# Kernel tuning notes

Hardware: AMD Instinct MI355X
Metric: run time of the kernel (lower is better)

The kernel has to match this reference:

```python
import jax, jax.numpy as jnp
import numpy as np

N = 50000   # nodes
E = 600000  # edges (avg degree ~12)
R = 8       # num_relations = 2 * n_speakers**2, n_speakers=2
B = 32      # num_bases = args.batch_size
GD, H1, H2 = 128, 128, 128


def setup_inputs() -> dict:
    key = jax.random.key(0)
    ks = jax.random.split(key, 16)
    w = lambda k, shape: jax.random.normal(k, shape, jnp.float32) * 0.05
    return {
        "node_features": jax.random.normal(ks[0], (N, GD), jnp.float32),
        "edge_index": jax.random.randint(ks[1], (2, E), 0, N),
        "edge_norm": jax.random.uniform(ks[2], (E,), jnp.float32),
        "edge_type": jax.random.randint(ks[3], (E,), 0, R),
        "basis": w(ks[4], (B, GD, H1)),
        "comp": w(ks[5], (R, B)),
        "root": w(ks[6], (GD, H1)),
        "bias1": jnp.zeros((H1,), jnp.float32),
        "w_key": w(ks[7], (H1, H2)),
        "b_key": jnp.zeros((H2,), jnp.float32),
        "w_query": w(ks[8], (H1, H2)),
        "b_query": jnp.zeros((H2,), jnp.float32),
        "w_value": w(ks[9], (H1, H2)),
        "b_value": jnp.zeros((H2,), jnp.float32),
        "w_skip": w(ks[10], (H1, H2)),
        "b_skip": jnp.zeros((H2,), jnp.float32),
    }


def reference(node_features, edge_index, edge_norm, edge_type, basis, comp,
              root, bias1, w_key, b_key, w_query, b_query, w_value, b_value,
              w_skip, b_skip):
    n = node_features.shape[0]
    r = comp.shape[0]
    src, dst = edge_index[0], edge_index[1]

    # ---- RGCNConv (basis decomposition, per-relation mean aggregation) ----
    W = jnp.einsum('rb,bio->rio', comp, basis)            # [R, GD, H1]
    xW = jnp.einsum('ni,rio->rno', node_features, W)      # [R, N, H1]
    msg = xW[edge_type, src]                              # [E, H1]
    seg = edge_type * n + dst                             # combined (relation, dst) segment id
    agg = jax.ops.segment_sum(msg, seg, num_segments=r * n).reshape(r, n, -1)
    cnt = jax.ops.segment_sum(jnp.ones(msg.shape[0], jnp.float32), seg,
                              num_segments=r * n).reshape(r, n, 1)
    h = (agg / jnp.maximum(cnt, 1.0)).sum(0) + node_features @ root + bias1

    # ---- ResGatedGraphConv: sigmoid(k_i + q_j) * v_j, sum-aggregated + skip ----
    k = h @ w_key + b_key
    q = h @ w_query + b_query
    v = h @ w_value + b_value
    m = jax.nn.sigmoid(k[dst] + q[src]) * v[src]          # [E, H2]
    out = jax.ops.segment_sum(m, dst, num_segments=n) + h @ w_skip + b_skip
    return out
```

## Files before the change

### kernel.cpp

```cpp
#include <hip/hip_runtime.h>
#include <stdint.h>

#define GD 128
#define H1 128
#define H2 128
#define NBASES 32
#define NREL 8
#define KA 1152

typedef __attribute__((ext_vector_type(8))) short bf16x8;
typedef __attribute__((ext_vector_type(4))) float f32x4;

static inline size_t align256(size_t x){ return (x + 255) & ~(size_t)255; }

__device__ __forceinline__ float bf2f(uint32_t u16){
  union { uint32_t u; float f; } c; c.u = (u16 & 0xffffu) << 16; return c.f;
}
__device__ __forceinline__ unsigned short f2bf(float f){
  union { float f; uint32_t u; } c; c.f = f;
  uint32_t u = c.u;
  u += 0x7fffu + ((u >> 16) & 1u);
  return (unsigned short)(u >> 16);
}
__device__ __forceinline__ uint32_t pkbf(float a, float b){
  union { float f; uint32_t u; } ca, cb; ca.f = a; cb.f = b;
  return __builtin_amdgcn_perm(cb.u + 0x8000u, ca.u + 0x8000u, 0x07060302u);
}
__device__ __forceinline__ float rdlanef(float v, int l){
  return __int_as_float(__builtin_amdgcn_readlane(__float_as_int(v), l));
}

__device__ __forceinline__ void async_copy16(void* lds_dst, const void* gsrc){
  __builtin_amdgcn_global_load_lds(
      (const __attribute__((address_space(1))) uint32_t*)gsrc,
      (__attribute__((address_space(3))) uint32_t*)lds_dst, 16, 0, 0);
}

__global__ void k_prep(const float* __restrict__ comp, const float* __restrict__ basis,
                       const float* __restrict__ root, unsigned short* __restrict__ Bht,
                       const float* __restrict__ wk, const float* __restrict__ wq,
                       const float* __restrict__ wv, const float* __restrict__ wsk,
                       const float* __restrict__ bk, const float* __restrict__ bq,
                       const float* __restrict__ bv, const float* __restrict__ bs,
                       unsigned short* __restrict__ B2t, float* __restrict__ Bb,
                       const float4* __restrict__ x, uint2* __restrict__ xout, int cnt4,
                       uint32_t* __restrict__ xpadz, int npadz,
                       const int* __restrict__ edst, const int* __restrict__ etyp,
                       int* __restrict__ cnt, int E, int n){
  const float LOG2E = 1.4426950408889634f;
  int b = blockIdx.x, t = threadIdx.x;
  if (b < 128){
    int i = b;
    int o = t & 127, rh = t >> 7;
    float bv[NBASES];
    #pragma unroll
    for (int bb = 0; bb < NBASES; ++bb)
      bv[bb] = basis[((size_t)bb*GD + i)*H1 + o];
    #pragma unroll
    for (int rr = 0; rr < 4; ++rr){
      int r = rh*4 + rr;
      float acc = 0.f;
      #pragma unroll
      for (int bb = 0; bb < NBASES; ++bb)
        acc += comp[r*NBASES + bb] * bv[bb];
      Bht[(size_t)o*KA + r*128 + i] = f2bf(acc);
    }
    if (rh == 1) Bht[(size_t)o*KA + 1024 + i] = f2bf(root[(size_t)i*H1 + o]);
  } else if (b < 128 + 256){
    int idx = (b - 128)*256 + t;
    int c = idx / H1, k = idx % H1;
    const float* w = (c < 128) ? wk : (c < 256) ? wq : (c < 384) ? wv : wsk;
    float val = w[(size_t)k*H2 + (c & 127)];
    if (c < 256) val *= LOG2E;
    B2t[idx] = f2bf(val);
    if (idx < 512){
      const float* bia = (idx < 128) ? bk : (idx < 256) ? bq : (idx < 384) ? bv : bs;
      float bval = bia[idx & 127];
      if (idx < 256) bval *= LOG2E;
      Bb[idx] = bval;
    }
  } else {
    int cb = b - (128 + 256);
    int ncastb = (cnt4 + 1023) >> 10;
    if (cb < ncastb){
      int base = cb*1024 + t;
      #pragma unroll
      for (int u = 0; u < 4; ++u){
        int i = base + u*256;
        if (i < cnt4){
          float4 v = x[i];
          uint2 o; o.x = pkbf(v.x, v.y); o.y = pkbf(v.z, v.w);
          xout[i] = o;
        }
      }
    } else if (cb < ncastb + 12){
      int i = (cb - ncastb)*256 + t;
      if (i < npadz) xpadz[i] = 0u;
    } else {
      int e = (cb - ncastb - 12)*256 + t;
      if (e < E) atomicAdd(&cnt[etyp[e]*n + edst[e]], 1);
    }
  }
}

__global__ void k_scanA(const int* __restrict__ deg, int* __restrict__ off,
                        int* __restrict__ btot, int len){
  __shared__ int wsum[16];
  int t = threadIdx.x, lane = t & 63, w = t >> 6;
  int i0 = blockIdx.x*8192 + t*8;
  int v[8];
  if (i0 + 7 < len){
    int4 va = *(const int4*)(deg + i0);
    int4 vb = *(const int4*)(deg + i0 + 4);
    v[0]=va.x; v[1]=va.y; v[2]=va.z; v[3]=va.w;
    v[4]=vb.x; v[5]=vb.y; v[6]=vb.z; v[7]=vb.w;
  } else {
    #pragma unroll
    for (int u = 0; u < 8; ++u) v[u] = (i0+u < len) ? deg[i0+u] : 0;
  }
  int s[8]; s[0] = v[0];
  #pragma unroll
  for (int u = 1; u < 8; ++u) s[u] = s[u-1] + v[u];
  int x = s[7];
  #pragma unroll
  for (int d = 1; d < 64; d <<= 1){
    int u = __shfl_up(x, d, 64);
    if (lane >= d) x += u;
  }
  if (lane == 63) wsum[w] = x;
  __syncthreads();
  if (t < 16){
    int y = wsum[t];
    #pragma unroll
    for (int d = 1; d < 16; d <<= 1){
      int u = __shfl_up(y, d, 16);
      if (t >= d) y += u;
    }
    wsum[t] = y;
  }
  __syncthreads();
  int woff = (w > 0) ? wsum[w-1] : 0;
  int excl = woff + x - s[7];
  #pragma unroll
  for (int u = 0; u < 8; ++u)
    if (i0+u < len) off[i0+u] = excl + s[u] - v[u];
  if (t == 0) btot[blockIdx.x] = wsum[15];
}

__global__ void k_scanB(const int* __restrict__ btot, int* __restrict__ off,
                        int* __restrict__ cursor, int len, int sentinel){
  int t = threadIdx.x, bid = blockIdx.x;
  int add = 0;
  for (int j = 0; j < bid; ++j) add += btot[j];
  int i0 = bid*8192 + t*8;
  #pragma unroll
  for (int u = 0; u < 8; ++u){
    int i = i0 + u;
    if (i < len){ int val = off[i] + add; off[i] = val; cursor[i] = val; }
  }
  if (bid == 0 && t == 0) off[len] = sentinel;
}

__global__ void k_scatter_rd(const int* __restrict__ src, const int* __restrict__ dst,
                             const int* __restrict__ typ, int* __restrict__ cursor,
                             int* __restrict__ pk, int E, int n){
  int e = blockIdx.x*blockDim.x + threadIdx.x;
  if (e >= E) return;
  int pos = atomicAdd(&cursor[typ[e]*n + dst[e]], 1);
  pk[pos] = src[e];
}

__launch_bounds__(256)
__global__ void k_fused(const int* __restrict__ off_rd, const int* __restrict__ pk_rd,
                        const uint32_t* __restrict__ x32, const unsigned short* __restrict__ xb,
                        const unsigned short* __restrict__ Bt, const float* __restrict__ bias1,
                        unsigned short* __restrict__ h, int n){
  __shared__ char lds[49152];
  int t = threadIdx.x, lane = t & 63, wave = t >> 6;
  int row0 = blockIdx.x * 128;
  int mrow = lane & 15, quad = lane >> 4;
  int wrow = (wave & 1) * 64, wcol = (wave >> 1) * 64;
  int s = (mrow >> 1) & 3;
  int colsw = (((t & 3) ^ ((t >> 3) & 3)) << 3);

  const unsigned short* Xsrc = xb + (size_t)(row0 + (t >> 2))*GD + colsw;
  const unsigned short* Bsrc = Bt + (size_t)(t >> 2)*KA + colsw;
  char* stage = lds + 32768;
  char* ldsw = stage + wave*1024;

  int aoff = (wrow + mrow)*64 + ((quad ^ s) << 4);
  int boff = 8192 + (wcol + mrow)*64 + ((quad ^ s) << 4);
  int axor = (mrow & 7) << 4;
  int wbase = wave*32;
  int d0 = row0 + wbase;

  f32x4 acc[4][4];
  #pragma unroll
  for (int i = 0; i < 4; ++i)
    #pragma unroll
    for (int j = 0; j < 4; ++j) acc[i][j] = (f32x4){0.f,0.f,0.f,0.f};

  for (int r = 0; r < 9; ++r){
    if (r < 8){
      __syncthreads();
      int oidx = d0 + lane; if (oidx > n) oidx = n;
      int ow = (lane < 33) ? off_rd[(size_t)r*n + oidx] : 0;
      int ownx = __shfl_down(ow, 1, 64);
      int cN = ownx - ow;
      float icN = (cN > 0) ? __builtin_amdgcn_rcpf((float)cN) : 0.f;
      int ebase = __builtin_amdgcn_readlane(ow, 0);
      int segN  = __builtin_amdgcn_readlane(ow, 32) - ebase;
      int pb[31];
      #pragma unroll
      for (int j = 0; j < 31; ++j)
        pb[j] = __builtin_amdgcn_readlane(ow, j + 1) - ebase;

      int cn = 0; float a0 = 0.f, a1 = 0.f;
#define TFLUSH(RK)                                                               \
      {                                                                          \
        float ic = rdlanef(icN, cn);                                             \
        *(uint32_t*)(lds + (wbase + cn)*256 + ((lane*4) ^ ((cn & 7) << 4)))      \
            = pkbf(a0*ic, a1*ic);                                                \
        for (int q2 = cn + 1; q2 < (RK); ++q2)                                   \
          *(uint32_t*)(lds + (wbase + q2)*256 + ((lane*4) ^ ((q2 & 7) << 4)))    \
              = 0u;                                                              \
        cn = (RK); a0 = 0.f; a1 = 0.f;                                           \
      }
      for (int jb = 0; jb < segN; jb += 64){
        int i = jb + lane;
        int node = 0;
        #pragma unroll
        for (int j = 0; j < 31; ++j) node += (i >= pb[j]);
        int m = segN - jb; if (m > 64) m = 64;
        int pj = (lane < m) ? pk_rd[ebase + i] : 0;
        int jj = 0;
        for (; jj + 8 <= m; jj += 8){
          uint32_t g[8];
          #pragma unroll
          for (int k = 0; k < 8; ++k){
            int sN = __builtin_amdgcn_readlane(pj, jj + k);
            g[k] = x32[(size_t)(uint32_t)sN*64 + lane];
          }
          #pragma unroll
          for (int k = 0; k < 8; ++k){
            int rk = __builtin_amdgcn_readlane(node, jj + k);
            if (rk != cn) TFLUSH(rk);
            a0 += bf2f(g[k]); a1 += bf2f(g[k] >> 16);
          }
        }
        for (; jj < m; jj += 4){
          int lim = m - 1;
          uint32_t g[4];
          #pragma unroll
          for (int k = 0; k < 4; ++k){
            int tt = jj + k; if (tt > lim) tt = lim;
            int sN = __builtin_amdgcn_readlane(pj, tt);
            g[k] = x32[(size_t)(uint32_t)sN*64 + lane];
          }
          #pragma unroll
          for (int k = 0; k < 4; ++k){
            int tt = jj + k;
            if (tt < m){
              int rk = __builtin_amdgcn_readlane(node, tt);
              if (rk != cn) TFLUSH(rk);
              a0 += bf2f(g[k]); a1 += bf2f(g[k] >> 16);
            }
          }
        }
      }
      TFLUSH(32)
#undef TFLUSH
      __syncthreads();
      for (int c4 = 0; c4 < 4; ++c4){
        int kts = c4*32;
        if (c4) __syncthreads();
        async_copy16(ldsw + 8192,  Bsrc + r*128 + kts);
        async_copy16(ldsw + 12288, Bsrc + (size_t)64*KA + r*128 + kts);
        __syncthreads();
        bf16x8 af[4], bf[4];
        #pragma unroll
        for (int i = 0; i < 4; ++i)
          af[i] = *(const bf16x8*)(lds + (wrow + i*16 + mrow)*256 + (((kts + quad*8)*2) ^ axor));
        #pragma unroll
        for (int j = 0; j < 4; ++j) bf[j] = *(const bf16x8*)(stage + boff + j*1024);
        #pragma unroll
        for (int i = 0; i < 4; ++i)
          #pragma unroll
          for (int j = 0; j < 4; ++j)
            acc[i][j] = __builtin_amdgcn_mfma_f32_16x16x32_bf16(af[i], bf[j], acc[i][j], 0, 0, 0);
      }
    } else {
      for (int c4 = 0; c4 < 4; ++c4){
        int kts = c4*32;
        __syncthreads();
        async_copy16(ldsw,         Xsrc + kts);
        async_copy16(ldsw + 4096,  Xsrc + (size_t)64*GD + kts);
        async_copy16(ldsw + 8192,  Bsrc + 1024 + kts);
        async_copy16(ldsw + 12288, Bsrc + (size_t)64*KA + 1024 + kts);
        __syncthreads();
        bf16x8 af[4], bf[4];
        #pragma unroll
        for (int i = 0; i < 4; ++i) af[i] = *(const bf16x8*)(stage + aoff + i*1024);
        #pragma unroll
        for (int j = 0; j < 4; ++j) bf[j] = *(const bf16x8*)(stage + boff + j*1024);
        #pragma unroll
        for (int i = 0; i < 4; ++i)
          #pragma unroll
          for (int j = 0; j < 4; ++j)
            acc[i][j] = __builtin_amdgcn_mfma_f32_16x16x32_bf16(af[i], bf[j], acc[i][j], 0, 0, 0);
      }
    }
  }
  float bc[4];
  #pragma unroll
  for (int j = 0; j < 4; ++j) bc[j] = bias1[wcol + j*16 + mrow];
  #pragma unroll
  for (int p = 0; p < 2; ++p){
    __syncthreads();
    if ((wave & 1) == p){
      #pragma unroll
      for (int j = 0; j < 4; ++j){
        int col = wcol + j*16 + mrow;
        #pragma unroll
        for (int i = 0; i < 4; ++i)
          #pragma unroll
          for (int rg = 0; rg < 4; ++rg){
            int rl = i*16 + quad*4 + rg;
            *(unsigned short*)(lds + rl*264 + col*2) = f2bf(acc[i][j][rg] + bc[j]);
          }
      }
    }
    __syncthreads();
    uint32_t vv[16];
    #pragma unroll
    for (int u = 0; u < 8; ++u)
      *(uint2*)&vv[u*2] = *(const uint2*)(lds + lane*264 + wave*64 + u*8);
    unsigned short* gp = h + (size_t)(row0 + p*64 + lane)*H1 + wave*32;
    #pragma unroll
    for (int u = 0; u < 4; ++u)
      *(uint4*)(gp + u*8) = *(const uint4*)&vv[u*4];
  }
}

__launch_bounds__(256)
__global__ void k_gemm2(const unsigned short* __restrict__ A, const unsigned short* __restrict__ Bt,
                        const float* __restrict__ Bb, unsigned short* __restrict__ kqv,
                        unsigned short* __restrict__ skipb){
  __shared__ char lds[16896];
  int t = threadIdx.x, lane = t & 63, wave = t >> 6;
  int row0 = blockIdx.x * 128;
  int c0 = blockIdx.y * 128;
  int mrow = lane & 15, quad = lane >> 4;
  int wrow = (wave & 1) * 64, wcol = (wave >> 1) * 64;
  int s = (mrow >> 1) & 3;

  const unsigned short* Asrc = A + (size_t)(row0 + (t >> 2))*H1 + (((t & 3) ^ ((t >> 3) & 3)) << 3);
  const unsigned short* Bsrc = Bt + (size_t)(c0 + (t >> 2))*H1 + (((t & 3) ^ ((t >> 3) & 3)) << 3);
  char* ldsw = lds + wave*1024;

  int aoff = (wrow + mrow)*64 + ((quad ^ s) << 4);
  int boff = 8192 + (wcol + mrow)*64 + ((quad ^ s) << 4);

  f32x4 acc[4][4];
  #pragma unroll
  for (int i = 0; i < 4; ++i)
    #pragma unroll
    for (int j = 0; j < 4; ++j) acc[i][j] = (f32x4){0.f,0.f,0.f,0.f};

  #pragma unroll
  for (int kt = 0; kt < H1; kt += 32){
    __syncthreads();
    async_copy16(ldsw,         Asrc + kt);
    async_copy16(ldsw + 4096,  Asrc + (size_t)64*H1 + kt);
    async_copy16(ldsw + 8192,  Bsrc + kt);
    async_copy16(ldsw + 12288, Bsrc + (size_t)64*H1 + kt);
    __syncthreads();
    bf16x8 af[4], bf[4];
    #pragma unroll
    for (int i = 0; i < 4; ++i) af[i] = *(const bf16x8*)(lds + aoff + i*1024);
    #pragma unroll
    for (int j = 0; j < 4; ++j) bf[j] = *(const bf16x8*)(lds + boff + j*1024);
    #pragma unroll
    for (int i = 0; i < 4; ++i)
      #pragma unroll
      for (int j = 0; j < 4; ++j)
        acc[i][j] = __builtin_amdgcn_mfma_f32_16x16x32_bf16(af[i], bf[j], acc[i][j], 0, 0, 0);
  }
  float bc[4];
  #pragma unroll
  for (int j = 0; j < 4; ++j) bc[j] = Bb[c0 + wcol + j*16 + mrow];
  unsigned short* dstb; size_t ldu;
  if (c0 < 384){ dstb = kqv + c0; ldu = 384; } else { dstb = skipb; ldu = 128; }
  #pragma unroll
  for (int p = 0; p < 2; ++p){
    __syncthreads();
    if ((wave & 1) == p){
      #pragma unroll
      for (int j = 0; j < 4; ++j){
        int col = wcol + j*16 + mrow;
        #pragma unroll
        for (int i = 0; i < 4; ++i)
          #pragma unroll
          for (int rg = 0; rg < 4; ++rg){
            int rl = i*16 + quad*4 + rg;
            *(unsigned short*)(lds + rl*264 + col*2) = f2bf(acc[i][j][rg] + bc[j]);
          }
      }
    }
    __syncthreads();
    uint32_t vv[16];
    #pragma unroll
    for (int u = 0; u < 8; ++u)
      *(uint2*)&vv[u*2] = *(const uint2*)(lds + lane*264 + wave*64 + u*8);
    unsigned short* gp = dstb + (size_t)(row0 + p*64 + lane)*ldu + wave*32;
    #pragma unroll
    for (int u = 0; u < 4; ++u)
      *(uint4*)(gp + u*8) = *(const uint4*)&vv[u*4];
  }
}

__global__ void k_edge2(const int* __restrict__ off_rd, const int* __restrict__ pk_rd,
                        const unsigned short* __restrict__ kqv,
                        const unsigned short* __restrict__ skipb,
                        float* __restrict__ out, int n){
  int wid = blockIdx.x*(blockDim.x >> 6) + (threadIdx.x >> 6);
  int lane = threadIdx.x & 63;
  if (wid >= n) return;
  const uint32_t* kv32 = (const uint32_t*)kqv;
  int r = lane & 7;
  int o_r = off_rd[(size_t)r*n + wid];
  int e_r = off_rd[(size_t)r*n + wid + 1];
  int c_r = e_r - o_r;
  int c0_ = __builtin_amdgcn_readlane(c_r, 0), c1_ = __builtin_amdgcn_readlane(c_r, 1);
  int c2_ = __builtin_amdgcn_readlane(c_r, 2), c3_ = __builtin_amdgcn_readlane(c_r, 3);
  int c4_ = __builtin_amdgcn_readlane(c_r, 4), c5_ = __builtin_amdgcn_readlane(c_r, 5);
  int c6_ = __builtin_amdgcn_readlane(c_r, 6), c7_ = __builtin_amdgcn_readlane(c_r, 7);
  int o0_ = __builtin_amdgcn_readlane(o_r, 0), o1_ = __builtin_amdgcn_readlane(o_r, 1);
  int o2_ = __builtin_amdgcn_readlane(o_r, 2), o3_ = __builtin_amdgcn_readlane(o_r, 3);
  int o4_ = __builtin_amdgcn_readlane(o_r, 4), o5_ = __builtin_amdgcn_readlane(o_r, 5);
  int o6_ = __builtin_amdgcn_readlane(o_r, 6), o7_ = __builtin_amdgcn_readlane(o_r, 7);
  int p1 = c0_, p2 = p1 + c1_, p3 = p2 + c2_, p4 = p3 + c3_;
  int p5 = p4 + c4_, p6 = p5 + c5_, p7 = p6 + c6_, dg = p7 + c7_;

  uint32_t ku = kv32[(size_t)wid*192 + lane];
  float k0 = bf2f(ku), k1 = bf2f(ku >> 16);
  float a0 = 0.f, a1 = 0.f;
  for (int jb = 0; jb < dg; jb += 64){
    int i = jb + lane;
    int adj = o0_;
    adj = (i >= p1) ? (o1_ - p1) : adj;
    adj = (i >= p2) ? (o2_ - p2) : adj;
    adj = (i >= p3) ? (o3_ - p3) : adj;
    adj = (i >= p4) ? (o4_ - p4) : adj;
    adj = (i >= p5) ? (o5_ - p5) : adj;
    adj = (i >= p6) ? (o6_ - p6) : adj;
    adj = (i >= p7) ? (o7_ - p7) : adj;
    int m = dg - jb; if (m > 64) m = 64;
    int pj = (lane < m) ? pk_rd[adj + i] : 0;
    int jj = 0;
    for (; jj + 8 <= m; jj += 8){
      uint32_t qg[8], vg[8];
      #pragma unroll
      for (int k = 0; k < 8; ++k){
        int s = __builtin_amdgcn_readlane(pj, jj + k);
        const uint32_t* rowp = kv32 + (size_t)s*192 + lane;
        qg[k] = rowp[64];
        vg[k] = rowp[128];
      }
      #pragma unroll
      for (int k = 0; k < 8; ++k){
        float qq0 = bf2f(qg[k]), qq1 = bf2f(qg[k] >> 16);
        float vv0 = bf2f(vg[k]), vv1 = bf2f(vg[k] >> 16);
        float g0 = __builtin_amdgcn_rcpf(1.f + __builtin_amdgcn_exp2f(-(k0 + qq0)));
        float g1 = __builtin_amdgcn_rcpf(1.f + __builtin_amdgcn_exp2f(-(k1 + qq1)));
        a0 += g0*vv0; a1 += g1*vv1;
      }
    }
    for (; jj + 4 <= m; jj += 4){
      uint32_t qg[4], vg[4];
      #pragma unroll
      for (int k = 0; k < 4; ++k){
        int s = __builtin_amdgcn_readlane(pj, jj + k);
        const uint32_t* rowp = kv32 + (size_t)s*192 + lane;
        qg[k] = rowp[64];
        vg[k] = rowp[128];
      }
      #pragma unroll
      for (int k = 0; k < 4; ++k){
        float qq0 = bf2f(qg[k]), qq1 = bf2f(qg[k] >> 16);
        float vv0 = bf2f(vg[k]), vv1 = bf2f(vg[k] >> 16);
        float g0 = __builtin_amdgcn_rcpf(1.f + __builtin_amdgcn_exp2f(-(k0 + qq0)));
        float g1 = __builtin_amdgcn_rcpf(1.f + __builtin_amdgcn_exp2f(-(k1 + qq1)));
        a0 += g0*vv0; a1 += g1*vv1;
      }
    }
    for (; jj < m; ++jj){
      int s = __builtin_amdgcn_readlane(pj, jj);
      const uint32_t* rowp = kv32 + (size_t)s*192 + lane;
      uint32_t qg = rowp[64], vg = rowp[128];
      float qq0 = bf2f(qg), qq1 = bf2f(qg >> 16);
      float vv0 = bf2f(vg), vv1 = bf2f(vg >> 16);
      float g0 = __builtin_amdgcn_rcpf(1.f + __builtin_amdgcn_exp2f(-(k0 + qq0)));
      float g1 = __builtin_amdgcn_rcpf(1.f + __builtin_amdgcn_exp2f(-(k1 + qq1)));
      a0 += g0*vv0; a1 += g1*vv1;
    }
  }
  uint32_t sk = ((const uint32_t*)skipb)[(size_t)wid*64 + lane];
  float2 cur; cur.x = a0 + bf2f(sk); cur.y = a1 + bf2f(sk >> 16);
  ((float2*)(out + (size_t)wid*H2))[lane] = cur;
}

extern "C" void kernel_launch(void* const* d_in, const int* in_sizes, int n_in,
                              void* d_out, int out_size, void* d_ws, size_t ws_size,
                              hipStream_t stream){
  const float* x     = (const float*)d_in[0];
  const int*   eidx  = (const int*)  d_in[1];
  const int*   etype = (const int*)  d_in[3];
  const float* basis = (const float*)d_in[4];
  const float* comp  = (const float*)d_in[5];
  const float* root  = (const float*)d_in[6];
  const float* bias1 = (const float*)d_in[7];
  const float* wk    = (const float*)d_in[8];
  const float* bk    = (const float*)d_in[9];
  const float* wq    = (const float*)d_in[10];
  const float* bq    = (const float*)d_in[11];
  const float* wv    = (const float*)d_in[12];
  const float* bv    = (const float*)d_in[13];
  const float* wsk   = (const float*)d_in[14];
  const float* bs    = (const float*)d_in[15];
  const int n = in_sizes[0] / GD;
  const int E = in_sizes[3];
  const int npad = (n + 127) & ~127;
  const int* esrc = eidx;
  const int* edst = eidx + E;
  float* out = (float*)d_out;

  char* w = (char*)d_ws;
  size_t off = 0;
  unsigned short* xbf  = (unsigned short*)(w + off); off = align256(off + (size_t)npad*GD*2);
  unsigned short* Bht  = (unsigned short*)(w + off); off = align256(off + (size_t)KA*H1*2);
  unsigned short* B2t  = (unsigned short*)(w + off); off = align256(off + (size_t)512*H1*2);
  float* Bb            = (float*)(w + off);          off = align256(off + 512*4);
  unsigned short* hbuf = (unsigned short*)(w + off); off = align256(off + (size_t)npad*H1*2);
  unsigned short* kqv  = (unsigned short*)(w + off); off = align256(off + (size_t)npad*384*2);
  unsigned short* skipb= (unsigned short*)(w + off); off = align256(off + (size_t)npad*H2*2);
  int* cnt_rd          = (int*)(w + off);            off = align256(off + (size_t)(8*n+4)*4);
  int* off_rd          = (int*)(w + off);            off = align256(off + (size_t)(8*n+1)*4);
  int* cur_rd          = (int*)(w + off);            off = align256(off + (size_t)8*n*4);
  int* btot_rd         = (int*)(w + off);            off = align256(off + 64*4);
  int* pk_rd           = (int*)(w + off);            off = align256(off + (size_t)E*4);

  const int nblk_rd = (8*n + 8191) / 8192;
  const int cnt4 = n*GD/4;
  const int ncastb = (cnt4 + 1023)/1024;
  const int histb  = (E + 255)/256;
  const int npadz  = (npad - n)*GD/2;

  hipMemsetAsync(cnt_rd, 0, (size_t)8*n*4, stream);

  k_prep<<<128 + 256 + ncastb + 12 + histb, 256, 0, stream>>>(
      comp, basis, root, Bht, wk, wq, wv, wsk, bk, bq, bv, bs, B2t, Bb,
      (const float4*)x, (uint2*)xbf, cnt4,
      (uint32_t*)(xbf + (size_t)n*GD), npadz,
      edst, etype, cnt_rd, E, n);
  k_scanA<<<nblk_rd, 1024, 0, stream>>>(cnt_rd, off_rd, btot_rd, 8*n);
  k_scanB<<<nblk_rd, 1024, 0, stream>>>(btot_rd, off_rd, cur_rd, 8*n, E);
  k_scatter_rd<<<(E + 255)/256, 256, 0, stream>>>(esrc, edst, etype, cur_rd, pk_rd, E, n);
  k_fused<<<npad/128, 256, 0, stream>>>(off_rd, pk_rd, (const uint32_t*)xbf, xbf,
                                        Bht, bias1, hbuf, n);
  k_gemm2<<<dim3(npad/128, 4), 256, 0, stream>>>(hbuf, B2t, Bb, kqv, skipb);
  k_edge2<<<(n + 3)/4, 256, 0, stream>>>(off_rd, pk_rd, kqv, skipb, out, n);
}
```

Baseline: 340.3 us.

## Halve fused RGCN block tile to 64 rows and prefetch full B slice per relation

The fused RGCN kernel now handles 64 destination rows per block instead of 128, with each wave gathering 16 nodes and computing a 64x32 output slab. The whole 128x128 weight slice for a relation is copied into LDS asynchronously before the gather phase, so the load overlaps the gather and the four per-chunk barriers go away. This doubles the grid for better occupancy and load balance. In exchange, each weight slice is reloaded by twice as many blocks and the kernel uses slightly more LDS.

After: 347.2 us. 2.0% more time.

```diff
diff --git a/kernel.cpp b/kernel.cpp
--- a/kernel.cpp
+++ b/kernel.cpp
@@ -175,44 +175,45 @@
                         const uint32_t* __restrict__ x32, const unsigned short* __restrict__ xb,
                         const unsigned short* __restrict__ Bt, const float* __restrict__ bias1,
                         unsigned short* __restrict__ h, int n){
-  __shared__ char lds[49152];
+  __shared__ char lds[49664];
   int t = threadIdx.x, lane = t & 63, wave = t >> 6;
-  int row0 = blockIdx.x * 128;
+  int row0 = blockIdx.x * 64;
   int mrow = lane & 15, quad = lane >> 4;
-  int wrow = (wave & 1) * 64, wcol = (wave >> 1) * 64;
   int s = (mrow >> 1) & 3;
   int colsw = (((t & 3) ^ ((t >> 3) & 3)) << 3);
 
   const unsigned short* Xsrc = xb + (size_t)(row0 + (t >> 2))*GD + colsw;
   const unsigned short* Bsrc = Bt + (size_t)(t >> 2)*KA + colsw;
-  char* stage = lds + 32768;
-  char* ldsw = stage + wave*1024;
-
-  int aoff = (wrow + mrow)*64 + ((quad ^ s) << 4);
-  int boff = 8192 + (wcol + mrow)*64 + ((quad ^ s) << 4);
+  char* Breg = lds + 16896;
+
   int axor = (mrow & 7) << 4;
-  int wbase = wave*32;
+  int wbase = wave*16;
   int d0 = row0 + wbase;
 
-  f32x4 acc[4][4];
+  f32x4 acc[4][2];
   #pragma unroll
   for (int i = 0; i < 4; ++i)
     #pragma unroll
-    for (int j = 0; j < 4; ++j) acc[i][j] = (f32x4){0.f,0.f,0.f,0.f};
+    for (int j = 0; j < 2; ++j) acc[i][j] = (f32x4){0.f,0.f,0.f,0.f};
 
   for (int r = 0; r < 9; ++r){
+    __syncthreads();
     if (r < 8){
-      __syncthreads();
+      #pragma unroll
+      for (int kk = 0; kk < 128; kk += 32){
+        async_copy16(Breg + (kk >> 5)*8192 + wave*1024,        Bsrc + r*128 + kk);
+        async_copy16(Breg + (kk >> 5)*8192 + wave*1024 + 4096, Bsrc + (size_t)64*KA + r*128 + kk);
+      }
       int oidx = d0 + lane; if (oidx > n) oidx = n;
-      int ow = (lane < 33) ? off_rd[(size_t)r*n + oidx] : 0;
+      int ow = (lane < 17) ? off_rd[(size_t)r*n + oidx] : 0;
       int ownx = __shfl_down(ow, 1, 64);
       int cN = ownx - ow;
       float icN = (cN > 0) ? __builtin_amdgcn_rcpf((float)cN) : 0.f;
       int ebase = __builtin_amdgcn_readlane(ow, 0);
-      int segN  = __builtin_amdgcn_readlane(ow, 32) - ebase;
-      int pb[31];
-      #pragma unroll
-      for (int j = 0; j < 31; ++j)
+      int segN  = __builtin_amdgcn_readlane(ow, 16) - ebase;
+      int pb[15];
+      #pragma unroll
+      for (int j = 0; j < 15; ++j)
         pb[j] = __builtin_amdgcn_readlane(ow, j + 1) - ebase;
 
       int cn = 0; float a0 = 0.f, a1 = 0.f;
@@ -230,7 +231,7 @@
         int i = jb + lane;
         int node = 0;
         #pragma unroll
-        for (int j = 0; j < 31; ++j) node += (i >= pb[j]);
+        for (int j = 0; j < 15; ++j) node += (i >= pb[j]);
         int m = segN - jb; if (m > 64) m = 64;
         int pj = (lane < m) ? pk_rd[ebase + i] : 0;
         int jj = 0;
@@ -268,78 +269,74 @@
           }
         }
       }
-      TFLUSH(32)
+      TFLUSH(16)
 #undef TFLUSH
       __syncthreads();
+      #pragma unroll
       for (int c4 = 0; c4 < 4; ++c4){
         int kts = c4*32;
-        if (c4) __syncthreads();
-        async_copy16(ldsw + 8192,  Bsrc + r*128 + kts);
-        async_copy16(ldsw + 12288, Bsrc + (size_t)64*KA + r*128 + kts);
-        __syncthreads();
-        bf16x8 af[4], bf[4];
+        bf16x8 af[4], bf[2];
         #pragma unroll
         for (int i = 0; i < 4; ++i)
-          af[i] = *(const bf16x8*)(lds + (wrow + i*16 + mrow)*256 + (((kts + quad*8)*2) ^ axor));
-        #pragma unroll
-        for (int j = 0; j < 4; ++j) bf[j] = *(const bf16x8*)(stage + boff + j*1024);
+          af[i] = *(const bf16x8*)(lds + (i*16 + mrow)*256 + (((kts + quad*8)*2) ^ axor));
+        #pragma unroll
+        for (int j = 0; j < 2; ++j)
+          bf[j] = *(const bf16x8*)(Breg + c4*8192 + (wave*32 + j*16 + mrow)*64 + ((quad ^ s) << 4));
         #pragma unroll
         for (int i = 0; i < 4; ++i)
           #pragma unroll
-          for (int j = 0; j < 4; ++j)
+          for (int j = 0; j < 2; ++j)
             acc[i][j] = __builtin_amdgcn_mfma_f32_16x16x32_bf16(af[i], bf[j], acc[i][j], 0, 0, 0);
       }
     } else {
+      #pragma unroll
+      for (int kk = 0; kk < 128; kk += 32){
+        async_copy16(lds  + (kk >> 5)*4096 + wave*1024,        Xsrc + kk);
+        async_copy16(Breg + (kk >> 5)*8192 + wave*1024,        Bsrc + 1024 + kk);
+        async_copy16(Breg + (kk >> 5)*8192 + wave*1024 + 4096, Bsrc + (size_t)64*KA + 1024 + kk);
+      }
+      __syncthreads();
+      #pragma unroll
       for (int c4 = 0; c4 < 4; ++c4){
-        int kts = c4*32;
-        __syncthreads();
-        async_copy16(ldsw,         Xsrc + kts);
-        async_copy16(ldsw + 4096,  Xsrc + (size_t)64*GD + kts);
-        async_copy16(ldsw + 8192,  Bsrc + 1024 + kts);
-        async_copy16(ldsw + 12288, Bsrc + (size_t)64*KA + 1024 + kts);
-        __syncthreads();
-        bf16x8 af[4], bf[4];
-        #pragma unroll
-        for (int i = 0; i < 4; ++i) af[i] = *(const bf16x8*)(stage + aoff + i*1024);
-        #pragma unroll
-        for (int j = 0; j < 4; ++j) bf[j] = *(const bf16x8*)(stage + boff + j*1024);
+        bf16x8 af[4], bf[2];
         #pragma unroll
         for (int i = 0; i < 4; ++i)
-          #pragma unroll
-          for (int j = 0; j < 4; ++j)
+          af[i] = *(const bf16x8*)(lds + c4*4096 + (i*16 + mrow)*64 + ((quad ^ s) << 4));
+        #pragma unroll
+        for (int j = 0; j < 2; ++j)
+          bf[j] = *(const bf16x8*)(Breg + c4*8192 + (wave*32 + j*16 + mrow)*64 + ((quad ^ s) << 4));
+        #pragma unroll
+        for (int i = 0; i < 4; ++i)
+          #pragma unroll
+          for (int j = 0; j < 2; ++j)
             acc[i][j] = __builtin_amdgcn_mfma_f32_16x16x32_bf16(af[i], bf[j], acc[i][j], 0, 0, 0);
       }
     }
   }
-  float bc[4];
-  #pragma unroll
-  for (int j = 0; j < 4; ++j) bc[j] = bias1[wcol + j*16 + mrow];
-  #pragma unroll
-  for (int p = 0; p < 2; ++p){
-    __syncthreads();
-    if ((wave & 1) == p){
-      #pragma unroll
-      for (int j = 0; j < 4; ++j){
-        int col = wcol + j*16 + mrow;
-        #pragma unroll
-        for (int i = 0; i < 4; ++i)
-          #pragma unroll
-          for (int rg = 0; rg < 4; ++rg){
-            int rl = i*16 + quad*4 + rg;
-            *(unsigned short*)(lds + rl*264 + col*2) = f2bf(acc[i][j][rg] + bc[j]);
-          }
-      }
-    }
-    __syncthreads();
-    uint32_t vv[16];
-    #pragma unroll
-    for (int u = 0; u < 8; ++u)
-      *(uint2*)&vv[u*2] = *(const uint2*)(lds + lane*264 + wave*64 + u*8);
-    unsigned short* gp = h + (size_t)(row0 + p*64 + lane)*H1 + wave*32;
-    #pragma unroll
-    for (int u = 0; u < 4; ++u)
-      *(uint4*)(gp + u*8) = *(const uint4*)&vv[u*4];
-  }
+  float bc[2];
+  #pragma unroll
+  for (int j = 0; j < 2; ++j) bc[j] = bias1[wave*32 + j*16 + mrow];
+  __syncthreads();
+  #pragma unroll
+  for (int j = 0; j < 2; ++j){
+    int col = wave*32 + j*16 + mrow;
+    #pragma unroll
+    for (int i = 0; i < 4; ++i)
+      #pragma unroll
+      for (int rg = 0; rg < 4; ++rg){
+        int rl = i*16 + quad*4 + rg;
+        *(unsigned short*)(lds + rl*264 + col*2) = f2bf(acc[i][j][rg] + bc[j]);
+      }
+  }
+  __syncthreads();
+  uint32_t vv[16];
+  #pragma unroll
+  for (int u = 0; u < 8; ++u)
+    *(uint2*)&vv[u*2] = *(const uint2*)(lds + lane*264 + wave*64 + u*8);
+  unsigned short* gp = h + (size_t)(row0 + lane)*H1 + wave*32;
+  #pragma unroll
+  for (int u = 0; u < 4; ++u)
+    *(uint4*)(gp + u*8) = *(const uint4*)&vv[u*4];
 }
 
 __launch_bounds__(256)
@@ -566,8 +563,8 @@
   k_scanA<<<nblk_rd, 1024, 0, stream>>>(cnt_rd, off_rd, btot_rd, 8*n);
   k_scanB<<<nblk_rd, 1024, 0, stream>>>(btot_rd, off_rd, cur_rd, 8*n, E);
   k_scatter_rd<<<(E + 255)/256, 256, 0, stream>>>(esrc, edst, etype, cur_rd, pk_rd, E, n);
-  k_fused<<<npad/128, 256, 0, stream>>>(off_rd, pk_rd, (const uint32_t*)xbf, xbf,
-                                        Bht, bias1, hbuf, n);
+  k_fused<<<npad/64, 256, 0, stream>>>(off_rd, pk_rd, (const uint32_t*)xbf, xbf,
+                                       Bht, bias1, hbuf, n);
   k_gemm2<<<dim3(npad/128, 4), 256, 0, stream>>>(hbuf, B2t, Bb, kqv, skipb);
   k_edge2<<<(n + 3)/4, 256, 0, stream>>>(off_rd, pk_rd, kqv, skipb, out, n);
 }
```

## Use 8 waves per block in fused RGCN kernel, halving rows per wave

Applied to the files above, without the earlier changes.

Doubles the fused aggregation+GEMM kernel's block size from 256 to 512 threads. Each wave now gathers 16 destination rows per relation instead of 32 and computes a 32x64 MFMA tile instead of 64x64, with staging and write-back remapped to match. The goal is more memory-level parallelism and latency hiding in the gather-heavy phase. The cost is more barrier participants, lower per-wave MFMA reuse, and possible register pressure under the 512-thread launch bound.

Result: slower. 358.2 us (+5.2%).

```diff
diff --git a/kernel.cpp b/kernel.cpp
--- a/kernel.cpp
+++ b/kernel.cpp
@@ -170,7 +170,7 @@
   pk[pos] = src[e];
 }
 
-__launch_bounds__(256)
+__launch_bounds__(512)
 __global__ void k_fused(const int* __restrict__ off_rd, const int* __restrict__ pk_rd,
                         const uint32_t* __restrict__ x32, const unsigned short* __restrict__ xb,
                         const unsigned short* __restrict__ Bt, const float* __restrict__ bias1,
@@ -179,41 +179,36 @@
   int t = threadIdx.x, lane = t & 63, wave = t >> 6;
   int row0 = blockIdx.x * 128;
   int mrow = lane & 15, quad = lane >> 4;
-  int wrow = (wave & 1) * 64, wcol = (wave >> 1) * 64;
   int s = (mrow >> 1) & 3;
   int colsw = (((t & 3) ^ ((t >> 3) & 3)) << 3);
 
   const unsigned short* Xsrc = xb + (size_t)(row0 + (t >> 2))*GD + colsw;
   const unsigned short* Bsrc = Bt + (size_t)(t >> 2)*KA + colsw;
-  char* stage = lds + 32768;
-  char* ldsw = stage + wave*1024;
-
-  int aoff = (wrow + mrow)*64 + ((quad ^ s) << 4);
-  int boff = 8192 + (wcol + mrow)*64 + ((quad ^ s) << 4);
+  char* Astage = lds + 32768;
+  char* Bstage = lds + 40960;
+
+  int wrow = (wave & 3) * 32;
+  int wcol = (wave >> 2) * 64;
   int axor = (mrow & 7) << 4;
-  int wbase = wave*32;
+  int wbase = wave*16;
   int d0 = row0 + wbase;
 
-  f32x4 acc[4][4];
-  #pragma unroll
-  for (int i = 0; i < 4; ++i)
+  f32x4 acc[2][4];
+  #pragma unroll
+  for (int i = 0; i < 2; ++i)
     #pragma unroll
     for (int j = 0; j < 4; ++j) acc[i][j] = (f32x4){0.f,0.f,0.f,0.f};
 
   for (int r = 0; r < 9; ++r){
+    __syncthreads();
     if (r < 8){
-      __syncthreads();
       int oidx = d0 + lane; if (oidx > n) oidx = n;
-      int ow = (lane < 33) ? off_rd[(size_t)r*n + oidx] : 0;
+      int ow = (lane < 17) ? off_rd[(size_t)r*n + oidx] : 0;
       int ownx = __shfl_down(ow, 1, 64);
       int cN = ownx - ow;
       float icN = (cN > 0) ? __builtin_amdgcn_rcpf((float)cN) : 0.f;
       int ebase = __builtin_amdgcn_readlane(ow, 0);
-      int segN  = __builtin_amdgcn_readlane(ow, 32) - ebase;
-      int pb[31];
-      #pragma unroll
-      for (int j = 0; j < 31; ++j)
-        pb[j] = __builtin_amdgcn_readlane(ow, j + 1) - ebase;
+      int segN  = __builtin_amdgcn_readlane(ow, 16) - ebase;
 
       int cn = 0; float a0 = 0.f, a1 = 0.f;
 #define TFLUSH(RK)                                                               \
@@ -230,7 +225,8 @@
         int i = jb + lane;
         int node = 0;
         #pragma unroll
-        for (int j = 0; j < 31; ++j) node += (i >= pb[j]);
+        for (int j = 0; j < 15; ++j)
+          node += (i >= (__builtin_amdgcn_readlane(ow, j + 1) - ebase));
         int m = segN - jb; if (m > 64) m = 64;
         int pj = (lane < m) ? pk_rd[ebase + i] : 0;
         int jj = 0;
@@ -268,23 +264,23 @@
           }
         }
       }
-      TFLUSH(32)
+      TFLUSH(16)
 #undef TFLUSH
       __syncthreads();
       for (int c4 = 0; c4 < 4; ++c4){
         int kts = c4*32;
         if (c4) __syncthreads();
-        async_copy16(ldsw + 8192,  Bsrc + r*128 + kts);
-        async_copy16(ldsw + 12288, Bsrc + (size_t)64*KA + r*128 + kts);
+        async_copy16(Bstage + wave*1024, Bsrc + r*128 + kts);
         __syncthreads();
-        bf16x8 af[4], bf[4];
-        #pragma unroll
-        for (int i = 0; i < 4; ++i)
+        bf16x8 af[2], bf[4];
+        #pragma unroll
+        for (int i = 0; i < 2; ++i)
           af[i] = *(const bf16x8*)(lds + (wrow + i*16 + mrow)*256 + (((kts + quad*8)*2) ^ axor));
         #pragma unroll
-        for (int j = 0; j < 4; ++j) bf[j] = *(const bf16x8*)(stage + boff + j*1024);
-        #pragma unroll
-        for (int i = 0; i < 4; ++i)
+        for (int j = 0; j < 4; ++j)
+          bf[j] = *(const bf16x8*)(Bstage + (wcol + j*16 + mrow)*64 + ((quad ^ s) << 4));
+        #pragma unroll
+        for (int i = 0; i < 2; ++i)
           #pragma unroll
           for (int j = 0; j < 4; ++j)
             acc[i][j] = __builtin_amdgcn_mfma_f32_16x16x32_bf16(af[i], bf[j], acc[i][j], 0, 0, 0);
@@ -292,19 +288,19 @@
     } else {
       for (int c4 = 0; c4 < 4; ++c4){
         int kts = c4*32;
+        if (c4) __syncthreads();
+        async_copy16(Astage + wave*1024, Xsrc + kts);
+        async_copy16(Bstage + wave*1024, Bsrc + 1024 + kts);
         __syncthreads();
-        async_copy16(ldsw,         Xsrc + kts);
-        async_copy16(ldsw + 4096,  Xsrc + (size_t)64*GD + kts);
-        async_copy16(ldsw + 8192,  Bsrc + 1024 + kts);
-        async_copy16(ldsw + 12288, Bsrc + (size_t)64*KA + 1024 + kts);
-        __syncthreads();
-        bf16x8 af[4], bf[4];
-        #pragma unroll
-        for (int i = 0; i < 4; ++i) af[i] = *(const bf16x8*)(stage + aoff + i*1024);
-        #pragma unroll
-        for (int j = 0; j < 4; ++j) bf[j] = *(const bf16x8*)(stage + boff + j*1024);
-        #pragma unroll
-        for (int i = 0; i < 4; ++i)
+        bf16x8 af[2], bf[4];
+        #pragma unroll
+        for (int i = 0; i < 2; ++i)
+          af[i] = *(const bf16x8*)(Astage + (wrow + i*16 + mrow)*64 + ((quad ^ s) << 4));
+        #pragma unroll
+        for (int j = 0; j < 4; ++j)
+          bf[j] = *(const bf16x8*)(Bstage + (wcol + j*16 + mrow)*64 + ((quad ^ s) << 4));
+        #pragma unroll
+        for (int i = 0; i < 2; ++i)
           #pragma unroll
           for (int j = 0; j < 4; ++j)
             acc[i][j] = __builtin_amdgcn_mfma_f32_16x16x32_bf16(af[i], bf[j], acc[i][j], 0, 0, 0);
@@ -317,28 +313,30 @@
   #pragma unroll
   for (int p = 0; p < 2; ++p){
     __syncthreads();
-    if ((wave & 1) == p){
+    if (((wave & 3) >> 1) == p){
+      int rbase = (wave & 3)*32 - p*64;
       #pragma unroll
       for (int j = 0; j < 4; ++j){
         int col = wcol + j*16 + mrow;
         #pragma unroll
-        for (int i = 0; i < 4; ++i)
+        for (int i = 0; i < 2; ++i)
           #pragma unroll
           for (int rg = 0; rg < 4; ++rg){
-            int rl = i*16 + quad*4 + rg;
+            int rl = rbase + i*16 + quad*4 + rg;
             *(unsigned short*)(lds + rl*264 + col*2) = f2bf(acc[i][j][rg] + bc[j]);
           }
       }
     }
     __syncthreads();
-    uint32_t vv[16];
-    #pragma unroll
-    for (int u = 0; u < 8; ++u)
-      *(uint2*)&vv[u*2] = *(const uint2*)(lds + lane*264 + wave*64 + u*8);
-    unsigned short* gp = h + (size_t)(row0 + p*64 + lane)*H1 + wave*32;
-    #pragma unroll
-    for (int u = 0; u < 4; ++u)
-      *(uint4*)(gp + u*8) = *(const uint4*)&vv[u*4];
+    uint2 v0 = *(const uint2*)(lds + lane*264 + wave*32);
+    uint2 v1 = *(const uint2*)(lds + lane*264 + wave*32 + 8);
+    uint2 v2 = *(const uint2*)(lds + lane*264 + wave*32 + 16);
+    uint2 v3 = *(const uint2*)(lds + lane*264 + wave*32 + 24);
+    unsigned short* gp = h + (size_t)(row0 + p*64 + lane)*H1 + wave*16;
+    uint4 o0; o0.x = v0.x; o0.y = v0.y; o0.z = v1.x; o0.w = v1.y;
+    uint4 o1; o1.x = v2.x; o1.y = v2.y; o1.z = v3.x; o1.w = v3.y;
+    *(uint4*)(gp)     = o0;
+    *(uint4*)(gp + 8) = o1;
   }
 }
 
@@ -566,7 +564,7 @@
   k_scanA<<<nblk_rd, 1024, 0, stream>>>(cnt_rd, off_rd, btot_rd, 8*n);
   k_scanB<<<nblk_rd, 1024, 0, stream>>>(btot_rd, off_rd, cur_rd, 8*n, E);
   k_scatter_rd<<<(E + 255)/256, 256, 0, stream>>>(esrc, edst, etype, cur_rd, pk_rd, E, n);
-  k_fused<<<npad/128, 256, 0, stream>>>(off_rd, pk_rd, (const uint32_t*)xbf, xbf,
+  k_fused<<<npad/128, 512, 0, stream>>>(off_rd, pk_rd, (const uint32_t*)xbf, xbf,
                                         Bht, bias1, hbuf, n);
   k_gemm2<<<dim3(npad/128, 4), 256, 0, stream>>>(hbuf, B2t, Bb, kqv, skipb);
   k_edge2<<<(n + 3)/4, 256, 0, stream>>>(off_rd, pk_rd, kqv, skipb, out, n);
```

## Split fused RGCN kernel across relation groups with fp32 partial reduction

Applied to the files above, without the earlier changes.

Splits the per-relation loop of the fused aggregation+GEMM kernel into three blockIdx.y groups (relations 0-2, 3-5, 6-7 plus root), so three times as many blocks run concurrently over 391 row tiles. Each group writes fp32 partial accumulators to a new workspace buffer, and a new reduction kernel sums them, adds bias1 and converts to bf16 h. The aim is better GPU occupancy on a grid too small to fill the device, at the cost of extra global traffic for the partials (about 77MB written and read) and one more launch.

Result: slower. 348.2 us (+2.3%).

```diff
diff --git a/kernel.cpp b/kernel.cpp
--- a/kernel.cpp
+++ b/kernel.cpp
@@ -173,11 +173,12 @@
 __launch_bounds__(256)
 __global__ void k_fused(const int* __restrict__ off_rd, const int* __restrict__ pk_rd,
                         const uint32_t* __restrict__ x32, const unsigned short* __restrict__ xb,
-                        const unsigned short* __restrict__ Bt, const float* __restrict__ bias1,
-                        unsigned short* __restrict__ h, int n){
+                        const unsigned short* __restrict__ Bt,
+                        float* __restrict__ hpart, int n, int npad){
   __shared__ char lds[49152];
   int t = threadIdx.x, lane = t & 63, wave = t >> 6;
   int row0 = blockIdx.x * 128;
+  int g = blockIdx.y;
   int mrow = lane & 15, quad = lane >> 4;
   int wrow = (wave & 1) * 64, wcol = (wave >> 1) * 64;
   int s = (mrow >> 1) & 3;
@@ -200,7 +201,8 @@
     #pragma unroll
     for (int j = 0; j < 4; ++j) acc[i][j] = (f32x4){0.f,0.f,0.f,0.f};
 
-  for (int r = 0; r < 9; ++r){
+  for (int u = 0; u < 3; ++u){
+    int r = g*3 + u;
     if (r < 8){
       __syncthreads();
       int oidx = d0 + lane; if (oidx > n) oidx = n;
@@ -235,27 +237,27 @@
         int pj = (lane < m) ? pk_rd[ebase + i] : 0;
         int jj = 0;
         for (; jj + 8 <= m; jj += 8){
-          uint32_t g[8];
+          uint32_t gg[8];
           #pragma unroll
           for (int k = 0; k < 8; ++k){
             int sN = __builtin_amdgcn_readlane(pj, jj + k);
-            g[k] = x32[(size_t)(uint32_t)sN*64 + lane];
+            gg[k] = x32[(size_t)(uint32_t)sN*64 + lane];
           }
           #pragma unroll
           for (int k = 0; k < 8; ++k){
             int rk = __builtin_amdgcn_readlane(node, jj + k);
             if (rk != cn) TFLUSH(rk);
-            a0 += bf2f(g[k]); a1 += bf2f(g[k] >> 16);
+            a0 += bf2f(gg[k]); a1 += bf2f(gg[k] >> 16);
           }
         }
         for (; jj < m; jj += 4){
           int lim = m - 1;
-          uint32_t g[4];
+          uint32_t gg[4];
           #pragma unroll
           for (int k = 0; k < 4; ++k){
             int tt = jj + k; if (tt > lim) tt = lim;
             int sN = __builtin_amdgcn_readlane(pj, tt);
-            g[k] = x32[(size_t)(uint32_t)sN*64 + lane];
+            gg[k] = x32[(size_t)(uint32_t)sN*64 + lane];
           }
           #pragma unroll
           for (int k = 0; k < 4; ++k){
@@ -263,7 +265,7 @@
             if (tt < m){
               int rk = __builtin_amdgcn_readlane(node, tt);
               if (rk != cn) TFLUSH(rk);
-              a0 += bf2f(g[k]); a1 += bf2f(g[k] >> 16);
+              a0 += bf2f(gg[k]); a1 += bf2f(gg[k] >> 16);
             }
           }
         }
@@ -311,35 +313,32 @@
       }
     }
   }
-  float bc[4];
-  #pragma unroll
-  for (int j = 0; j < 4; ++j) bc[j] = bias1[wcol + j*16 + mrow];
-  #pragma unroll
-  for (int p = 0; p < 2; ++p){
-    __syncthreads();
-    if ((wave & 1) == p){
-      #pragma unroll
-      for (int j = 0; j < 4; ++j){
-        int col = wcol + j*16 + mrow;
-        #pragma unroll
-        for (int i = 0; i < 4; ++i)
-          #pragma unroll
-          for (int rg = 0; rg < 4; ++rg){
-            int rl = i*16 + quad*4 + rg;
-            *(unsigned short*)(lds + rl*264 + col*2) = f2bf(acc[i][j][rg] + bc[j]);
-          }
-      }
-    }
-    __syncthreads();
-    uint32_t vv[16];
-    #pragma unroll
-    for (int u = 0; u < 8; ++u)
-      *(uint2*)&vv[u*2] = *(const uint2*)(lds + lane*264 + wave*64 + u*8);
-    unsigned short* gp = h + (size_t)(row0 + p*64 + lane)*H1 + wave*32;
-    #pragma unroll
-    for (int u = 0; u < 4; ++u)
-      *(uint4*)(gp + u*8) = *(const uint4*)&vv[u*4];
-  }
+  float* hp = hpart + (size_t)g*npad*H1;
+  #pragma unroll
+  for (int j = 0; j < 4; ++j){
+    int col = wcol + j*16 + mrow;
+    #pragma unroll
+    for (int i = 0; i < 4; ++i)
+      #pragma unroll
+      for (int rg = 0; rg < 4; ++rg){
+        int row = row0 + wrow + i*16 + quad*4 + rg;
+        hp[(size_t)row*H1 + col] = acc[i][j][rg];
+      }
+  }
+}
+
+__global__ void k_hred(const float* __restrict__ hpart, const float* __restrict__ bias1,
+                       unsigned short* __restrict__ h, int npad){
+  int i = blockIdx.x*blockDim.x + threadIdx.x;
+  size_t stride = (size_t)npad*H1;
+  float4 a = ((const float4*)hpart)[i];
+  float4 b = ((const float4*)(hpart + stride))[i];
+  float4 c = ((const float4*)(hpart + 2*stride))[i];
+  float4 bb = ((const float4*)bias1)[i & 31];
+  uint2 o;
+  o.x = pkbf(a.x + b.x + c.x + bb.x, a.y + b.y + c.y + bb.y);
+  o.y = pkbf(a.z + b.z + c.z + bb.z, a.w + b.w + c.w + bb.w);
+  ((uint2*)h)[i] = o;
 }
 
 __launch_bounds__(256)
@@ -542,6 +541,7 @@
   unsigned short* B2t  = (unsigned short*)(w + off); off = align256(off + (size_t)512*H1*2);
   float* Bb            = (float*)(w + off);          off = align256(off + 512*4);
   unsigned short* hbuf = (unsigned short*)(w + off); off = align256(off + (size_t)npad*H1*2);
+  float* hpart         = (float*)(w + off);          off = align256(off + (size_t)3*npad*H1*4);
   unsigned short* kqv  = (unsigned short*)(w + off); off = align256(off + (size_t)npad*384*2);
   unsigned short* skipb= (unsigned short*)(w + off); off = align256(off + (size_t)npad*H2*2);
   int* cnt_rd          = (int*)(w + off);            off = align256(off + (size_t)(8*n+4)*4);
@@ -566,8 +566,9 @@
   k_scanA<<<nblk_rd, 1024, 0, stream>>>(cnt_rd, off_rd, btot_rd, 8*n);
   k_scanB<<<nblk_rd, 1024, 0, stream>>>(btot_rd, off_rd, cur_rd, 8*n, E);
   k_scatter_rd<<<(E + 255)/256, 256, 0, stream>>>(esrc, edst, etype, cur_rd, pk_rd, E, n);
-  k_fused<<<npad/128, 256, 0, stream>>>(off_rd, pk_rd, (const uint32_t*)xbf, xbf,
-                                        Bht, bias1, hbuf, n);
+  k_fused<<<dim3(npad/128, 3), 256, 0, stream>>>(off_rd, pk_rd, (const uint32_t*)xbf, xbf,
+                                                 Bht, hpart, n, npad);
+  k_hred<<<npad*H1/4/256, 256, 0, stream>>>(hpart, bias1, hbuf, npad);
   k_gemm2<<<dim3(npad/128, 4), 256, 0, stream>>>(hbuf, B2t, Bb, kqv, skipb);
   k_edge2<<<(n + 3)/4, 256, 0, stream>>>(off_rd, pk_rd, kqv, skipb, out, n);
 }
```
